# Optimization experiments

Hardware: AMD Instinct MI355X
Metric: run time of the kernel (lower is better)

The kernel has to match this reference:

```python
import jax, jax.numpy as jnp
import numpy as np

N_USER = 100000
N_ITEM = 100000
N_TAG = 10000
DIM = 128
E_BUYS = 1_000_000
E_REV = 1_000_000
E_TAGS = 1_000_000
W_SCALE = 0.05


def setup_inputs() -> dict:
    key = jax.random.key(0)
    ks = jax.random.split(key, 18)
    inp = {
        "x_user": jax.random.normal(ks[0], (N_USER, DIM), jnp.float32),
        "x_item": jax.random.normal(ks[1], (N_ITEM, DIM), jnp.float32),
        "x_tag": jax.random.normal(ks[2], (N_TAG, DIM), jnp.float32),
        # edge_index per relation: row 0 = src node ids, row 1 = dst node ids
        "ei_buys": jnp.stack([
            jax.random.randint(ks[3], (E_BUYS,), 0, N_USER, jnp.int32),
            jax.random.randint(ks[4], (E_BUYS,), 0, N_ITEM, jnp.int32)]),
        "ei_rev": jnp.stack([
            jax.random.randint(ks[5], (E_REV,), 0, N_ITEM, jnp.int32),
            jax.random.randint(ks[6], (E_REV,), 0, N_USER, jnp.int32)]),
        "ei_tags": jnp.stack([
            jax.random.randint(ks[7], (E_TAGS,), 0, N_TAG, jnp.int32),
            jax.random.randint(ks[8], (E_TAGS,), 0, N_ITEM, jnp.int32)]),
    }
    # SAGEConv params per edge type: lin_l (neighbor agg), lin_r (root), bias
    names = ["buys", "rev", "tags"]
    for i, n in enumerate(names):
        inp[f"Wl_{n}"] = jax.random.normal(ks[9 + 3 * i], (DIM, DIM), jnp.float32) * W_SCALE
        inp[f"Wr_{n}"] = jax.random.normal(ks[10 + 3 * i], (DIM, DIM), jnp.float32) * W_SCALE
        inp[f"b_{n}"] = jnp.zeros((DIM,), jnp.float32)
    return inp


def _sage(x_src, x_dst, ei, Wl, Wr, b):
    """SAGEConv with mean neighbor aggregation: lin_l(mean_j x_j) + lin_r(x_i) + b."""
    n_dst = x_dst.shape[0]
    src, dst = ei[0], ei[1]
    msg_sum = jax.ops.segment_sum(x_src[src], dst, num_segments=n_dst)  # [n_dst, D]
    cnt = jax.ops.segment_sum(jnp.ones(src.shape, x_src.dtype), dst, num_segments=n_dst)
    msg_mean = msg_sum / jnp.maximum(cnt, 1.0)[:, None]
    return msg_mean @ Wl + x_dst @ Wr + b


def reference(x_user, x_item, x_tag, ei_buys, ei_rev, ei_tags,
              Wl_buys, Wr_buys, b_buys,
              Wl_rev, Wr_rev, b_rev,
              Wl_tags, Wr_tags, b_tags):
    # per-relation SAGEConv
    o_item_buys = _sage(x_user, x_item, ei_buys, Wl_buys, Wr_buys, b_buys)
    o_user = _sage(x_item, x_user, ei_rev, Wl_rev, Wr_rev, b_rev)
    o_item_tags = _sage(x_tag, x_item, ei_tags, Wl_tags, Wr_tags, b_tags)
    # HeteroConv aggr='mean' across edge types per destination node type
    out_item = 0.5 * (o_item_buys + o_item_tags)
    out_user = o_user  # single relation into 'user'
    return (out_user, out_item)
```

## Files before the change

### kernel.cpp

```cpp
#include <hip/hip_runtime.h>
#include <hip/hip_bf16.h>
#include <stdint.h>

#define DIM 128
#define NNODE 100000
#define NB 98
#define NBT (3 * NB)
#define T_TILE 8192

typedef __attribute__((ext_vector_type(8))) short short8;
typedef __attribute__((ext_vector_type(4))) float f32x4;

__device__ __forceinline__ unsigned short f32_to_bf16_rne(float f) {
    union { float f; uint32_t u; } v; v.f = f;
    uint32_t u = v.u;
    uint32_t r = u + 0x7FFFu + ((u >> 16) & 1u);
    return (unsigned short)(r >> 16);
}
__device__ __forceinline__ float bf16_to_f32(unsigned short u) {
    union { uint32_t i; float f; } v; v.i = ((uint32_t)u) << 16; return v.f;
}

__global__ __launch_bounds__(256) void coarse_hist(
    const int* __restrict__ ei0, const int* __restrict__ ei1, const int* __restrict__ ei2,
    int E0, int E1, int E2, int* __restrict__ ccnt) {
    __shared__ int h[NBT];
    int Etot = E0 + E1 + E2;
    for (int i = threadIdx.x; i < NBT; i += 256) h[i] = 0;
    __syncthreads();
    for (int e = blockIdx.x * blockDim.x + threadIdx.x; e < Etot; e += gridDim.x * blockDim.x) {
        int rel, le; const int* ei; int E;
        if (e < E0)           { rel = 0; le = e;           ei = ei0; E = E0; }
        else if (e < E0 + E1) { rel = 1; le = e - E0;      ei = ei1; E = E1; }
        else                  { rel = 2; le = e - E0 - E1; ei = ei2; E = E2; }
        int d = ei[E + le];
        atomicAdd(&h[rel * NB + (d >> 10)], 1);
    }
    __syncthreads();
    for (int i = threadIdx.x; i < NBT; i += 256) {
        int c = h[i];
        if (c) atomicAdd(&ccnt[i], c);
    }
}

__global__ __launch_bounds__(512) void coarse_scan(const int* __restrict__ ccnt,
                                                   int* __restrict__ bases,
                                                   int* __restrict__ cursor) {
    __shared__ int s[512];
    int t = threadIdx.x;
    int v = (t < NBT) ? ccnt[t] : 0;
    s[t] = v;
    __syncthreads();
    for (int d = 1; d < 512; d <<= 1) {
        int x = (t >= d) ? s[t - d] : 0;
        __syncthreads();
        s[t] += x;
        __syncthreads();
    }
    int excl = s[t] - v;
    if (t < NBT) { bases[t] = excl; cursor[t] = excl; }
    if (t == NBT) bases[NBT] = excl;
}

__global__ __launch_bounds__(256) void coarse_scatter(
    const int* __restrict__ ei0, const int* __restrict__ ei1, const int* __restrict__ ei2,
    int E0, int E1, int E2, int* __restrict__ cursor, int* __restrict__ pairs) {
    __shared__ int h[NBT], hb[NBT], lc[NBT];
    int Etot = E0 + E1 + E2;
    int ntiles = (Etot + T_TILE - 1) / T_TILE;
    for (int tile = blockIdx.x; tile < ntiles; tile += gridDim.x) {
        int tbase = tile * T_TILE;
        for (int i = threadIdx.x; i < NBT; i += 256) { h[i] = 0; lc[i] = 0; }
        __syncthreads();
        int binreg[32], valreg[32];
        #pragma unroll
        for (int k = 0; k < 32; k++) {
            int e = tbase + k * 256 + threadIdx.x;
            binreg[k] = -1;
            if (e < Etot) {
                int rel, le; const int* ei; int E;
                if (e < E0)           { rel = 0; le = e;           ei = ei0; E = E0; }
                else if (e < E0 + E1) { rel = 1; le = e - E0;      ei = ei1; E = E1; }
                else                  { rel = 2; le = e - E0 - E1; ei = ei2; E = E2; }
                int d = ei[E + le];
                int s = ei[le];
                int bin = rel * NB + (d >> 10);
                binreg[k] = bin;
                valreg[k] = s | ((d & 1023) << 17);
                atomicAdd(&h[bin], 1);
            }
        }
        __syncthreads();
        for (int i = threadIdx.x; i < NBT; i += 256) {
            int c = h[i];
            hb[i] = c ? atomicAdd(&cursor[i], c) : 0;
        }
        __syncthreads();
        #pragma unroll
        for (int k = 0; k < 32; k++) {
            if (binreg[k] >= 0) {
                int bin = binreg[k];
                int pos = hb[bin] + atomicAdd(&lc[bin], 1);
                pairs[pos] = valreg[k];
            }
        }
        __syncthreads();
    }
}

__global__ __launch_bounds__(256) void fine_sort(
    const int* __restrict__ bases, const int* __restrict__ pairs,
    int* __restrict__ off, int* __restrict__ sorted, int N) {
    __shared__ int h[1024], ho[1024], ssum[256];
    int b = blockIdx.x;
    int rel = b / NB, jb = b - rel * NB;
    int ebase = bases[b], ne = bases[b + 1] - ebase;
    int dbase = jb << 10;
    int tid = threadIdx.x;
    for (int i = tid; i < 1024; i += 256) h[i] = 0;
    __syncthreads();
    for (int i = tid; i < ne; i += 256) {
        int dl = pairs[ebase + i] >> 17;
        atomicAdd(&h[dl], 1);
    }
    __syncthreads();
    int v0 = h[tid * 4], v1 = h[tid * 4 + 1], v2 = h[tid * 4 + 2], v3 = h[tid * 4 + 3];
    int tsum = v0 + v1 + v2 + v3;
    ssum[tid] = tsum;
    __syncthreads();
    for (int s = 1; s < 256; s <<= 1) {
        int t = (tid >= s) ? ssum[tid - s] : 0;
        __syncthreads();
        ssum[tid] += t;
        __syncthreads();
    }
    int excl = ssum[tid] - tsum;
    ho[tid * 4] = excl;
    ho[tid * 4 + 1] = excl + v0;
    ho[tid * 4 + 2] = excl + v0 + v1;
    ho[tid * 4 + 3] = excl + v0 + v1 + v2;
    __syncthreads();
    for (int i = tid; i < 1024; i += 256) {
        int d = dbase + i;
        if (d < N) off[rel * N + d] = ebase + ho[i];
        h[i] = 0;
    }
    __syncthreads();
    for (int i = tid; i < ne; i += 256) {
        int p = pairs[ebase + i];
        int dl = p >> 17;
        int pos = ebase + ho[dl] + atomicAdd(&h[dl], 1);
        sorted[pos] = p & 0x1FFFF;
    }
}

__global__ void pack_kernel(const float* __restrict__ Wl_b, const float* __restrict__ Wr_b,
                            const float* __restrict__ b_b,
                            const float* __restrict__ Wl_r, const float* __restrict__ Wr_r,
                            const float* __restrict__ b_r,
                            const float* __restrict__ Wl_t, const float* __restrict__ Wr_t,
                            const float* __restrict__ b_t,
                            unsigned short* __restrict__ pw_item,
                            unsigned short* __restrict__ pw_user,
                            float* __restrict__ bias_item, float* __restrict__ bias_user) {
    const int NI = 12 * 8 * 64 * 8;
    const int NU = 8 * 8 * 64 * 8;
    int o = blockIdx.x * blockDim.x + threadIdx.x;
    if (o < NI) {
        int j = o & 7, lane = (o >> 3) & 63, ks = o >> 12;
        int n = ((o >> 9) & 7) * 16 + (lane & 15);
        int k = (ks & 3) * 32 + (lane >> 4) * 8 + j;
        int src = ks >> 2;
        float v;
        if (src == 0)      v = 0.5f * Wl_b[k * DIM + n];
        else if (src == 1) v = 0.5f * Wl_t[k * DIM + n];
        else               v = 0.5f * (Wr_b[k * DIM + n] + Wr_t[k * DIM + n]);
        pw_item[o] = f32_to_bf16_rne(v);
    } else if (o < NI + NU) {
        int oo = o - NI;
        int j = oo & 7, lane = (oo >> 3) & 63, ks = oo >> 12;
        int n = ((oo >> 9) & 7) * 16 + (lane & 15);
        int k = (ks & 3) * 32 + (lane >> 4) * 8 + j;
        float v = ((ks >> 2) == 0) ? Wl_r[k * DIM + n] : Wr_r[k * DIM + n];
        pw_user[oo] = f32_to_bf16_rne(v);
    } else {
        int oo = o - NI - NU;
        if (oo < DIM)            bias_item[oo] = 0.5f * (b_b[oo] + b_t[oo]);
        else if (oo < 2 * DIM)   bias_user[oo - DIM] = b_r[oo - DIM];
    }
}

__device__ __forceinline__ void cg_product(
    unsigned char* stage, const short8* af,
    const unsigned short* __restrict__ pw, int slot0,
    const float* __restrict__ bias,
    unsigned short* __restrict__ dst, int g0, int lane) {
    const int quad = lane >> 4, l15 = lane & 15;
    f32x4 acc[8];
    #pragma unroll
    for (int i = 0; i < 8; i++) acc[i] = (f32x4){0.f, 0.f, 0.f, 0.f};
    #pragma unroll
    for (int ksl = 0; ksl < 4; ksl++) {
        const unsigned short* wp = pw + ((size_t)(slot0 + ksl) * 8 * 64 + lane) * 8;
        #pragma unroll
        for (int nt = 0; nt < 8; nt++) {
            short8 wfrag = *(const short8*)(wp + (size_t)nt * 64 * 8);
            acc[nt] = __builtin_amdgcn_mfma_f32_16x16x32_bf16(af[ksl], wfrag, acc[nt], 0, 0, 0);
        }
    }
    unsigned short* outb = (unsigned short*)stage;
    #pragma unroll
    for (int nt = 0; nt < 8; nt++) {
        float bv = bias ? bias[nt * 16 + l15] : 0.f;
        #pragma unroll
        for (int r = 0; r < 4; r++) {
            outb[(((quad << 2) + r) << 7) + (nt << 4) + l15] =
                f32_to_bf16_rne(acc[nt][r] + bv);
        }
    }
    unsigned char* mp = (unsigned char*)(dst + ((size_t)g0 << 7));
    #pragma unroll
    for (int s = 0; s < 4; s++) {
        uint4 vv = *(const uint4*)(stage + (s << 10) + (lane << 4));
        *(uint4*)(mp + (s << 10) + (lane << 4)) = vv;
    }
}

__global__ __launch_bounds__(256) void conv_gemm(
    const float* __restrict__ xu, const float* __restrict__ xi, const float* __restrict__ xt,
    const unsigned short* __restrict__ pw_item, const unsigned short* __restrict__ pw_user,
    const float* __restrict__ bias_item, const float* __restrict__ bias_user,
    unsigned short* __restrict__ yu, unsigned short* __restrict__ yi,
    unsigned short* __restrict__ yt,
    unsigned short* __restrict__ ru, unsigned short* __restrict__ ri,
    int GU, int GI, int GT) {
    __shared__ __align__(1024) unsigned char smem[4][4096];
    const int wid = threadIdx.x >> 6;
    const int lane = threadIdx.x & 63;
    const int grp = blockIdx.x * 4 + wid;
    if (grp >= GU + GI + GT) return;
    const float* src; const unsigned short *pwA, *pwB; const float* biasB;
    unsigned short *outA, *outB; int slotA, slotB, g0; bool two;
    if (grp < GU) {
        g0 = grp << 4; src = xu + ((size_t)g0 << 7);
        pwA = pw_item; slotA = 0; outA = yu;
        pwB = pw_user; slotB = 4; outB = ru; biasB = bias_user; two = true;
    } else if (grp < GU + GI) {
        g0 = (grp - GU) << 4; src = xi + ((size_t)g0 << 7);
        pwA = pw_user; slotA = 0; outA = yi;
        pwB = pw_item; slotB = 8; outB = ri; biasB = bias_item; two = true;
    } else {
        g0 = (grp - GU - GI) << 4; src = xt + ((size_t)g0 << 7);
        pwA = pw_item; slotA = 4; outA = yt; two = false;
        pwB = nullptr; outB = nullptr; biasB = nullptr; slotB = 0;
    }
    unsigned char* stage = smem[wid];
    #pragma unroll
    for (int s = 0; s < 8; s++) {
        float4 f = *(const float4*)((const unsigned char*)src + (s << 10) + (lane << 4));
        int row = (s << 1) + (lane >> 5);
        unsigned int b = ((unsigned int)row << 8) + ((unsigned int)(lane & 31) << 3);
        b ^= (unsigned int)((row & 15) << 4);
        ushort4 u;
        u.x = f32_to_bf16_rne(f.x); u.y = f32_to_bf16_rne(f.y);
        u.z = f32_to_bf16_rne(f.z); u.w = f32_to_bf16_rne(f.w);
        *(ushort4*)(stage + b) = u;
    }
    short8 af[4];
    const int quad = lane >> 4, l15 = lane & 15;
    #pragma unroll
    for (int ksl = 0; ksl < 4; ksl++) {
        unsigned int rb = ((unsigned int)l15 << 8) + (ksl << 6) + (quad << 4);
        rb ^= (unsigned int)(l15 << 4);
        af[ksl] = *(const short8*)(stage + rb);
    }
    cg_product(stage, af, pwA, slotA, nullptr, outA, g0, lane);
    if (two) cg_product(stage, af, pwB, slotB, biasB, outB, g0, lane);
}

__device__ __forceinline__ void gather_seg(
    const unsigned short* __restrict__ xs, const int* __restrict__ sorted,
    const int* bnd, unsigned char* stage, unsigned char* segb,
    int lane, int Etot, f32x4* acc) {
    const int b0 = bnd[0];
    const int L  = bnd[16] - b0;
    if (L <= 0) return;
    int nchunk = (L + 31) >> 5;
    if (nchunk > 20) nchunk = 20;
    const int tot = nchunk << 5;
    for (int i = lane; i < tot; i += 64) {
        int k = b0 + i;
        int s = 0;
        #pragma unroll
        for (int t = 1; t <= 16; t++) s += (k >= bnd[t]) ? 1 : 0;
        segb[i] = (unsigned char)s;
    }
    const int l15 = lane & 15;
    int deg = bnd[l15 + 1] - bnd[l15];
    const short ivb = (short)f32_to_bf16_rne(1.0f / (float)max(deg, 1));
    const int jsel = (lane & 7) >> 1;
    const int laneoff = ((lane >> 3) << 5) + ((lane & 1) << 4);
    const unsigned int stage_u =
        (unsigned int)(size_t)(__attribute__((address_space(3))) unsigned char*)stage;
    const unsigned int tbA = stage_u + ((lane >> 4) << 11) + ((lane & 15) << 3);
    const unsigned char* xsb = (const unsigned char*)xs;
    const int kmax = min(b0 + L - 1, Etot - 1);
    for (int c = 0; c < nchunk; c++) {
        int kk = min(b0 + (c << 5) + (lane & 31), kmax);
        const int sv = sorted[kk];
        #pragma unroll
        for (int q = 0; q < 8; q++) {
            int srow = __shfl(sv, (q << 2) + jsel, 64);
            const unsigned char* gp = xsb + (((size_t)srow) << 8) + laneoff;
            __builtin_amdgcn_global_load_lds(
                (const __attribute__((address_space(1))) unsigned int*)gp,
                (__attribute__((address_space(3))) unsigned int*)(stage + (q << 10)),
                16, 0, 0);
        }
        const unsigned long long sg =
            *(const unsigned long long*)(segb + (c << 5) + ((lane >> 4) << 3));
        short8 af;
        #pragma unroll
        for (int j = 0; j < 8; j++)
            af[j] = ((int)((sg >> (j << 3)) & 0xFFull) == l15) ? ivb : (short)0;
        asm volatile("s_waitcnt vmcnt(0)" ::: "memory");
        unsigned long long blo[8], bhi[8];
        #pragma unroll
        for (int nt = 0; nt < 8; nt++) {
            asm volatile("ds_read_b64_tr_b16 %0, %2\n\t"
                         "ds_read_b64_tr_b16 %1, %2 offset:1024"
                         : "=&v"(blo[nt]), "=&v"(bhi[nt]) : "v"(tbA + (nt << 7)));
        }
        asm volatile("s_waitcnt lgkmcnt(0)" ::: "memory");
        __builtin_amdgcn_sched_barrier(0);
        #pragma unroll
        for (int nt = 0; nt < 8; nt++) {
            union { unsigned long long u[2]; short8 s; } cv;
            cv.u[0] = blo[nt]; cv.u[1] = bhi[nt];
            acc[nt] = __builtin_amdgcn_mfma_f32_16x16x32_bf16(af, cv.s, acc[nt], 0, 0, 0);
        }
    }
}

__global__ __launch_bounds__(256) void agg_final(
    const unsigned short* __restrict__ yu, const unsigned short* __restrict__ yi,
    const unsigned short* __restrict__ yt,
    const unsigned short* __restrict__ ru, const unsigned short* __restrict__ ri,
    const int* __restrict__ sorted, const int* __restrict__ off,
    float* __restrict__ out, int N, int Etot) {
    __shared__ __align__(1024) unsigned char smem[4][9216];
    const int wid = threadIdx.x >> 6;
    const int lane = threadIdx.x & 63;
    const int grp = blockIdx.x * 4 + wid;
    const int Gi = N >> 4;
    if (grp >= 2 * Gi) return;
    unsigned char* stage = smem[wid];
    unsigned char* segb  = smem[wid] + 8192;
    int* bnd = (int*)(smem[wid] + 8192 + 640);
    const int quad = lane >> 4, l15 = lane & 15;

    f32x4 acc[8];
    #pragma unroll
    for (int i = 0; i < 8; i++) acc[i] = (f32x4){0.f, 0.f, 0.f, 0.f};

    float* op; const unsigned short* rt; int g0;
    if (grp < Gi) {
        g0 = grp << 4;
        if (lane < 17) bnd[lane] = off[g0 + lane];
        gather_seg(yu, sorted, bnd, stage, segb, lane, Etot, acc);
        if (lane < 17) { int idx = 2 * N + g0 + lane; bnd[lane] = (idx < 3 * N) ? off[idx] : Etot; }
        gather_seg(yt, sorted, bnd, stage, segb, lane, Etot, acc);
        op = out + (size_t)N * DIM; rt = ri;
    } else {
        g0 = (grp - Gi) << 4;
        if (lane < 17) bnd[lane] = off[N + g0 + lane];
        gather_seg(yi, sorted, bnd, stage, segb, lane, Etot, acc);
        op = out; rt = ru;
    }
    #pragma unroll
    for (int nt = 0; nt < 8; nt++) {
        #pragma unroll
        for (int r = 0; r < 4; r++) {
            size_t idx = (size_t)(g0 + (quad << 2) + r) * DIM + (nt << 4) + l15;
            op[idx] = acc[nt][r] + bf16_to_f32(rt[idx]);
        }
    }
}

extern "C" void kernel_launch(void* const* d_in, const int* in_sizes, int n_in,
                              void* d_out, int out_size, void* d_ws, size_t ws_size,
                              hipStream_t stream) {
    const float* x_user = (const float*)d_in[0];
    const float* x_item = (const float*)d_in[1];
    const float* x_tag  = (const float*)d_in[2];
    const int* ei_buys  = (const int*)d_in[3];
    const int* ei_rev   = (const int*)d_in[4];
    const int* ei_tags  = (const int*)d_in[5];
    const float* Wl_b = (const float*)d_in[6];
    const float* Wr_b = (const float*)d_in[7];
    const float* b_b  = (const float*)d_in[8];
    const float* Wl_r = (const float*)d_in[9];
    const float* Wr_r = (const float*)d_in[10];
    const float* b_r  = (const float*)d_in[11];
    const float* Wl_t = (const float*)d_in[12];
    const float* Wr_t = (const float*)d_in[13];
    const float* b_t  = (const float*)d_in[14];

    const int N  = NNODE;
    const int E0 = in_sizes[3] / 2, E1 = in_sizes[4] / 2, E2 = in_sizes[5] / 2;
    const int n_user = in_sizes[0] / DIM, n_item = in_sizes[1] / DIM, n_tag = in_sizes[2] / DIM;

    char* w = (char*)d_ws;
    int* off    = (int*)(w + 0);
    int* ccnt   = (int*)(w + 1200128);
    int* bases  = (int*)(w + 1201408);
    int* cursor = (int*)(w + 1202688);
    int* sorted = (int*)(w + 1204224);
    int* pairs  = (int*)(w + 13204480);
    unsigned short* pw_item = (unsigned short*)(w + 25204736);
    unsigned short* pw_user = (unsigned short*)(w + 25303040);
    float* bias_item = (float*)(w + 25368576);
    float* bias_user = (float*)(w + 25369088);
    unsigned short* yu = (unsigned short*)(w + 25369856);
    unsigned short* yi = (unsigned short*)(w + 50969856);
    unsigned short* yt = (unsigned short*)(w + 76569856);
    unsigned short* ru = (unsigned short*)(w + 79129856);
    unsigned short* ri = (unsigned short*)(w + 104729856);

    float* out_all = (float*)d_out;

    int Etot = E0 + E1 + E2;

    hipMemsetAsync(ccnt, 0, NBT * sizeof(int), stream);

    pack_kernel<<<(49152 + 32768 + 2 * DIM + 255) / 256, 256, 0, stream>>>(
        Wl_b, Wr_b, b_b, Wl_r, Wr_r, b_r, Wl_t, Wr_t, b_t,
        pw_item, pw_user, bias_item, bias_user);

    int GU = n_user / 16, GI = n_item / 16, GT = n_tag / 16;
    conv_gemm<<<(GU + GI + GT + 3) / 4, 256, 0, stream>>>(
        x_user, x_item, x_tag, pw_item, pw_user, bias_item, bias_user,
        yu, yi, yt, ru, ri, GU, GI, GT);

    coarse_hist<<<512, 256, 0, stream>>>(ei_buys, ei_rev, ei_tags, E0, E1, E2, ccnt);

    coarse_scan<<<1, 512, 0, stream>>>(ccnt, bases, cursor);

    int ntiles = (Etot + T_TILE - 1) / T_TILE;
    coarse_scatter<<<ntiles, 256, 0, stream>>>(
        ei_buys, ei_rev, ei_tags, E0, E1, E2, cursor, pairs);

    fine_sort<<<NBT, 256, 0, stream>>>(bases, pairs, off, sorted, N);

    int ngrp = 2 * (N / 16);
    agg_final<<<(ngrp + 3) / 4, 256, 0, stream>>>(
        yu, yi, yt, ru, ri, sorted, off, out_all, N, Etot);
}
```

Before: 435.4 us.

## Replace two-level bucket sort with per-node degree histogram, scan, and atomic scatter

Replaces the coarse-bin/fine-sort CSR construction with a direct counting sort: global atomic degree histogram per destination node, a three-kernel prefix scan, and an atomic-cursor scatter of source ids. It removes the intermediate pairs buffer and the per-bin shared-memory sorting passes. In exchange it adds many contended global atomics (3M on histogram, 3M returning atomics on scatter), a larger memset, and extra scan launches, and edge order within a segment becomes nondeterministic.

```diff
diff --git a/kernel.cpp b/kernel.cpp
--- a/kernel.cpp
+++ b/kernel.cpp
@@ -4,9 +4,6 @@
 
 #define DIM 128
 #define NNODE 100000
-#define NB 98
-#define NBT (3 * NB)
-#define T_TILE 8192
 
 typedef __attribute__((ext_vector_type(8))) short short8;
 typedef __attribute__((ext_vector_type(4))) float f32x4;
@@ -21,34 +18,42 @@
     union { uint32_t i; float f; } v; v.i = ((uint32_t)u) << 16; return v.f;
 }
 
-__global__ __launch_bounds__(256) void coarse_hist(
+__global__ __launch_bounds__(256) void edge_hist(
     const int* __restrict__ ei0, const int* __restrict__ ei1, const int* __restrict__ ei2,
-    int E0, int E1, int E2, int* __restrict__ ccnt) {
-    __shared__ int h[NBT];
+    int E0, int E1, int E2, int* __restrict__ deg) {
     int Etot = E0 + E1 + E2;
-    for (int i = threadIdx.x; i < NBT; i += 256) h[i] = 0;
-    __syncthreads();
-    for (int e = blockIdx.x * blockDim.x + threadIdx.x; e < Etot; e += gridDim.x * blockDim.x) {
+    for (int e = blockIdx.x * 256 + threadIdx.x; e < Etot; e += gridDim.x * 256) {
         int rel, le; const int* ei; int E;
         if (e < E0)           { rel = 0; le = e;           ei = ei0; E = E0; }
         else if (e < E0 + E1) { rel = 1; le = e - E0;      ei = ei1; E = E1; }
         else                  { rel = 2; le = e - E0 - E1; ei = ei2; E = E2; }
-        int d = ei[E + le];
-        atomicAdd(&h[rel * NB + (d >> 10)], 1);
-    }
+        atomicAdd(&deg[rel * NNODE + ei[E + le]], 1);
+    }
+}
+
+__global__ __launch_bounds__(1024) void scan_a(const int* __restrict__ deg,
+                                               int* __restrict__ loc,
+                                               int* __restrict__ bsum, int n) {
+    __shared__ int s[1024];
+    int t = threadIdx.x;
+    int gid = blockIdx.x * 1024 + t;
+    int v = (gid < n) ? deg[gid] : 0;
+    s[t] = v;
     __syncthreads();
-    for (int i = threadIdx.x; i < NBT; i += 256) {
-        int c = h[i];
-        if (c) atomicAdd(&ccnt[i], c);
-    }
-}
-
-__global__ __launch_bounds__(512) void coarse_scan(const int* __restrict__ ccnt,
-                                                   int* __restrict__ bases,
-                                                   int* __restrict__ cursor) {
+    for (int d = 1; d < 1024; d <<= 1) {
+        int x = (t >= d) ? s[t - d] : 0;
+        __syncthreads();
+        s[t] += x;
+        __syncthreads();
+    }
+    if (gid < n) loc[gid] = s[t] - v;
+    if (t == 1023) bsum[blockIdx.x] = s[1023];
+}
+
+__global__ __launch_bounds__(512) void scan_b(int* __restrict__ bsum, int nb) {
     __shared__ int s[512];
     int t = threadIdx.x;
-    int v = (t < NBT) ? ccnt[t] : 0;
+    int v = (t < nb) ? bsum[t] : 0;
     s[t] = v;
     __syncthreads();
     for (int d = 1; d < 512; d <<= 1) {
@@ -57,100 +62,34 @@
         s[t] += x;
         __syncthreads();
     }
-    int excl = s[t] - v;
-    if (t < NBT) { bases[t] = excl; cursor[t] = excl; }
-    if (t == NBT) bases[NBT] = excl;
-}
-
-__global__ __launch_bounds__(256) void coarse_scatter(
+    if (t < nb) bsum[t] = s[t] - v;
+}
+
+__global__ __launch_bounds__(256) void scan_c(const int* __restrict__ loc,
+                                              const int* __restrict__ bsum,
+                                              int* __restrict__ off, int* __restrict__ cursor,
+                                              int n, int Etot) {
+    int i = blockIdx.x * 256 + threadIdx.x;
+    if (i < n) {
+        int o = loc[i] + bsum[i >> 10];
+        off[i] = o; cursor[i] = o;
+    }
+    if (i == n) off[n] = Etot;
+}
+
+__global__ __launch_bounds__(256) void edge_scatter(
     const int* __restrict__ ei0, const int* __restrict__ ei1, const int* __restrict__ ei2,
-    int E0, int E1, int E2, int* __restrict__ cursor, int* __restrict__ pairs) {
-    __shared__ int h[NBT], hb[NBT], lc[NBT];
+    int E0, int E1, int E2, int* __restrict__ cursor, int* __restrict__ sorted) {
     int Etot = E0 + E1 + E2;
-    int ntiles = (Etot + T_TILE - 1) / T_TILE;
-    for (int tile = blockIdx.x; tile < ntiles; tile += gridDim.x) {
-        int tbase = tile * T_TILE;
-        for (int i = threadIdx.x; i < NBT; i += 256) { h[i] = 0; lc[i] = 0; }
-        __syncthreads();
-        int binreg[32], valreg[32];
-        #pragma unroll
-        for (int k = 0; k < 32; k++) {
-            int e = tbase + k * 256 + threadIdx.x;
-            binreg[k] = -1;
-            if (e < Etot) {
-                int rel, le; const int* ei; int E;
-                if (e < E0)           { rel = 0; le = e;           ei = ei0; E = E0; }
-                else if (e < E0 + E1) { rel = 1; le = e - E0;      ei = ei1; E = E1; }
-                else                  { rel = 2; le = e - E0 - E1; ei = ei2; E = E2; }
-                int d = ei[E + le];
-                int s = ei[le];
-                int bin = rel * NB + (d >> 10);
-                binreg[k] = bin;
-                valreg[k] = s | ((d & 1023) << 17);
-                atomicAdd(&h[bin], 1);
-            }
-        }
-        __syncthreads();
-        for (int i = threadIdx.x; i < NBT; i += 256) {
-            int c = h[i];
-            hb[i] = c ? atomicAdd(&cursor[i], c) : 0;
-        }
-        __syncthreads();
-        #pragma unroll
-        for (int k = 0; k < 32; k++) {
-            if (binreg[k] >= 0) {
-                int bin = binreg[k];
-                int pos = hb[bin] + atomicAdd(&lc[bin], 1);
-                pairs[pos] = valreg[k];
-            }
-        }
-        __syncthreads();
-    }
-}
-
-__global__ __launch_bounds__(256) void fine_sort(
-    const int* __restrict__ bases, const int* __restrict__ pairs,
-    int* __restrict__ off, int* __restrict__ sorted, int N) {
-    __shared__ int h[1024], ho[1024], ssum[256];
-    int b = blockIdx.x;
-    int rel = b / NB, jb = b - rel * NB;
-    int ebase = bases[b], ne = bases[b + 1] - ebase;
-    int dbase = jb << 10;
-    int tid = threadIdx.x;
-    for (int i = tid; i < 1024; i += 256) h[i] = 0;
-    __syncthreads();
-    for (int i = tid; i < ne; i += 256) {
-        int dl = pairs[ebase + i] >> 17;
-        atomicAdd(&h[dl], 1);
-    }
-    __syncthreads();
-    int v0 = h[tid * 4], v1 = h[tid * 4 + 1], v2 = h[tid * 4 + 2], v3 = h[tid * 4 + 3];
-    int tsum = v0 + v1 + v2 + v3;
-    ssum[tid] = tsum;
-    __syncthreads();
-    for (int s = 1; s < 256; s <<= 1) {
-        int t = (tid >= s) ? ssum[tid - s] : 0;
-        __syncthreads();
-        ssum[tid] += t;
-        __syncthreads();
-    }
-    int excl = ssum[tid] - tsum;
-    ho[tid * 4] = excl;
-    ho[tid * 4 + 1] = excl + v0;
-    ho[tid * 4 + 2] = excl + v0 + v1;
-    ho[tid * 4 + 3] = excl + v0 + v1 + v2;
-    __syncthreads();
-    for (int i = tid; i < 1024; i += 256) {
-        int d = dbase + i;
-        if (d < N) off[rel * N + d] = ebase + ho[i];
-        h[i] = 0;
-    }
-    __syncthreads();
-    for (int i = tid; i < ne; i += 256) {
-        int p = pairs[ebase + i];
-        int dl = p >> 17;
-        int pos = ebase + ho[dl] + atomicAdd(&h[dl], 1);
-        sorted[pos] = p & 0x1FFFF;
+    for (int e = blockIdx.x * 256 + threadIdx.x; e < Etot; e += gridDim.x * 256) {
+        int rel, le; const int* ei; int E;
+        if (e < E0)           { rel = 0; le = e;           ei = ei0; E = E0; }
+        else if (e < E0 + E1) { rel = 1; le = e - E0;      ei = ei1; E = E1; }
+        else                  { rel = 2; le = e - E0 - E1; ei = ei2; E = E2; }
+        int d = ei[E + le];
+        int srcv = ei[le];
+        int pos = atomicAdd(&cursor[rel * NNODE + d], 1);
+        sorted[pos] = srcv;
     }
 }
 
@@ -368,7 +307,7 @@
         g0 = grp << 4;
         if (lane < 17) bnd[lane] = off[g0 + lane];
         gather_seg(yu, sorted, bnd, stage, segb, lane, Etot, acc);
-        if (lane < 17) { int idx = 2 * N + g0 + lane; bnd[lane] = (idx < 3 * N) ? off[idx] : Etot; }
+        if (lane < 17) { int idx = 2 * N + g0 + lane; bnd[lane] = (idx <= 3 * N) ? off[idx] : Etot; }
         gather_seg(yt, sorted, bnd, stage, segb, lane, Etot, acc);
         op = out + (size_t)N * DIM; rt = ri;
     } else {
@@ -409,29 +348,30 @@
     const int N  = NNODE;
     const int E0 = in_sizes[3] / 2, E1 = in_sizes[4] / 2, E2 = in_sizes[5] / 2;
     const int n_user = in_sizes[0] / DIM, n_item = in_sizes[1] / DIM, n_tag = in_sizes[2] / DIM;
+    const int n3 = 3 * N;
 
     char* w = (char*)d_ws;
     int* off    = (int*)(w + 0);
-    int* ccnt   = (int*)(w + 1200128);
-    int* bases  = (int*)(w + 1201408);
-    int* cursor = (int*)(w + 1202688);
-    int* sorted = (int*)(w + 1204224);
-    int* pairs  = (int*)(w + 13204480);
-    unsigned short* pw_item = (unsigned short*)(w + 25204736);
-    unsigned short* pw_user = (unsigned short*)(w + 25303040);
-    float* bias_item = (float*)(w + 25368576);
-    float* bias_user = (float*)(w + 25369088);
-    unsigned short* yu = (unsigned short*)(w + 25369856);
-    unsigned short* yi = (unsigned short*)(w + 50969856);
-    unsigned short* yt = (unsigned short*)(w + 76569856);
-    unsigned short* ru = (unsigned short*)(w + 79129856);
-    unsigned short* ri = (unsigned short*)(w + 104729856);
+    int* deg    = (int*)(w + 1200128);
+    int* cursor = (int*)(w + 2400256);
+    int* loc    = (int*)(w + 3600384);
+    int* bsum   = (int*)(w + 4800512);
+    int* sorted = (int*)(w + 4801792);
+    unsigned short* pw_item = (unsigned short*)(w + 16801792);
+    unsigned short* pw_user = (unsigned short*)(w + 16900096);
+    float* bias_item = (float*)(w + 16965632);
+    float* bias_user = (float*)(w + 16966144);
+    unsigned short* yu = (unsigned short*)(w + 16966656);
+    unsigned short* yi = (unsigned short*)(w + 42566656);
+    unsigned short* yt = (unsigned short*)(w + 68166656);
+    unsigned short* ru = (unsigned short*)(w + 70726656);
+    unsigned short* ri = (unsigned short*)(w + 96326656);
 
     float* out_all = (float*)d_out;
 
     int Etot = E0 + E1 + E2;
 
-    hipMemsetAsync(ccnt, 0, NBT * sizeof(int), stream);
+    hipMemsetAsync(deg, 0, (size_t)n3 * sizeof(int), stream);
 
     pack_kernel<<<(49152 + 32768 + 2 * DIM + 255) / 256, 256, 0, stream>>>(
         Wl_b, Wr_b, b_b, Wl_r, Wr_r, b_r, Wl_t, Wr_t, b_t,
@@ -442,15 +382,14 @@
         x_user, x_item, x_tag, pw_item, pw_user, bias_item, bias_user,
         yu, yi, yt, ru, ri, GU, GI, GT);
 
-    coarse_hist<<<512, 256, 0, stream>>>(ei_buys, ei_rev, ei_tags, E0, E1, E2, ccnt);
-
-    coarse_scan<<<1, 512, 0, stream>>>(ccnt, bases, cursor);
-
-    int ntiles = (Etot + T_TILE - 1) / T_TILE;
-    coarse_scatter<<<ntiles, 256, 0, stream>>>(
-        ei_buys, ei_rev, ei_tags, E0, E1, E2, cursor, pairs);
-
-    fine_sort<<<NBT, 256, 0, stream>>>(bases, pairs, off, sorted, N);
+    edge_hist<<<2048, 256, 0, stream>>>(ei_buys, ei_rev, ei_tags, E0, E1, E2, deg);
+
+    int nblkA = (n3 + 1023) / 1024;
+    scan_a<<<nblkA, 1024, 0, stream>>>(deg, loc, bsum, n3);
+    scan_b<<<1, 512, 0, stream>>>(bsum, nblkA);
+    scan_c<<<(n3 + 1 + 255) / 256, 256, 0, stream>>>(loc, bsum, off, cursor, n3, Etot);
+
+    edge_scatter<<<2048, 256, 0, stream>>>(ei_buys, ei_rev, ei_tags, E0, E1, E2, cursor, sorted);
 
     int ngrp = 2 * (N / 16);
     agg_final<<<(ngrp + 3) / 4, 256, 0, stream>>>(
```

Result: slower. 720.9 us (+65.6%).
